# Optimization experiments

Measured on AMD Instinct MI355X. Metric: run time of the kernel, lower is better.

The kernel has to match this reference:

```python
import jax, jax.numpy as jnp
from jax import lax
import numpy as np

N_GROUP = 1024   # number of FPS centroids
N_SAMPLE = 32    # neighbors per ball query
RADIUS = 0.2
BN_EPS = 1e-5    # torch BatchNorm2d default, training-mode batch stats
MLP = [64, 64, 128]
IN_CH = 6        # 3 relative xyz + 3 point features


def setup_inputs() -> dict:
    key = jax.random.key(0)
    ks = jax.random.split(key, 8)
    B, N = 16, 4096
    out = {
        "xyz": jax.random.uniform(ks[0], (B, N, 3), dtype=jnp.float32),
        "point_feature": jax.random.normal(ks[1], (B, N, 3), dtype=jnp.float32),
    }
    last = IN_CH
    for li, oc in enumerate(MLP):
        out[f"w{li}"] = jax.random.normal(ks[2 + li], (oc, last), dtype=jnp.float32) / np.float32(np.sqrt(last))
        out[f"b{li}"] = jnp.zeros((oc,), jnp.float32)
        out[f"g{li}"] = jnp.ones((oc,), jnp.float32)
        out[f"be{li}"] = jnp.zeros((oc,), jnp.float32)
        last = oc
    return out


def _fps(xyz, n_group):
    # Farthest point sampling. xyz: [B, N, 3] -> idx [B, n_group]
    B, N, _ = xyz.shape

    def step(carry, _):
        dist, farthest = carry                      # [B,N], [B]
        centroid = jnp.take_along_axis(xyz, farthest[:, None, None], axis=1)  # [B,1,3]
        d = jnp.sum((xyz - centroid) ** 2, -1)      # [B,N]
        dist = jnp.minimum(dist, d)
        nxt = jnp.argmax(dist, -1).astype(jnp.int32)
        return (dist, nxt), farthest

    init = (jnp.full((B, N), 1e10, xyz.dtype), jnp.zeros((B,), jnp.int32))
    _, idxs = lax.scan(step, init, None, length=n_group)
    return idxs.T                                    # [B, n_group]


def _ball_query(xyz, new_xyz, radius, n_sample):
    # xyz: [B,N,3], new_xyz: [B,S,3] -> idx [B,S,n_sample]
    B, N, _ = xyz.shape
    sqr = jnp.sum((new_xyz[:, :, None, :] - xyz[:, None, :, :]) ** 2, -1)  # [B,S,N]
    idx = jnp.where(sqr > radius * radius, N, jnp.arange(N, dtype=jnp.int32))
    idx = jnp.sort(idx, axis=-1)[:, :, :n_sample]    # closest-index fill like torch impl
    first = idx[:, :, :1]
    return jnp.where(idx == N, first, idx)


def reference(xyz, point_feature, w0, b0, g0, be0, w1, b1, g1, be1, w2, b2, g2, be2):
    B = xyz.shape[0]
    fps_idx = _fps(xyz, N_GROUP)                     # [B,S]
    bi = jnp.arange(B)[:, None]
    new_xyz = xyz[bi, fps_idx]                       # [B,S,3]

    idx = _ball_query(xyz, new_xyz, RADIUS, N_SAMPLE)  # [B,S,K]
    bii = jnp.arange(B)[:, None, None]
    grouped_xyz = xyz[bii, idx] - new_xyz[:, :, None, :]   # [B,S,K,3] centered
    grouped_feat = point_feature[bii, idx]                 # [B,S,K,3]
    x = jnp.concatenate([grouped_xyz, grouped_feat], -1)   # [B,S,K,6]

    # 1x1 Conv2d == per-point linear; BN over all dims but channel (training stats)
    for w, b, g, be in ((w0, b0, g0, be0), (w1, b1, g1, be1), (w2, b2, g2, be2)):
        x = jnp.einsum('bskc,oc->bsko', x, w) + b
        mu = x.mean((0, 1, 2))
        var = x.var((0, 1, 2))
        x = g * (x - mu) * lax.rsqrt(var + BN_EPS) + be
        x = jax.nn.relu(x)

    new_feature = x.max(axis=2)                      # max over n_sample -> [B,S,128]
    return new_xyz, new_feature
```

## Files before the change

kernel.cpp:

```cpp
#include <hip/hip_runtime.h>
#include <hip/hip_bf16.h>

constexpr int BATCH = 16;
constexpr int NPT   = 4096;
constexpr int NGRP  = 1024;
constexpr int NSMP  = 32;
constexpr int NPTS  = BATCH * NGRP * NSMP;
constexpr int PBLK  = 4096;
constexpr int NG    = BATCH * NGRP;

__device__ __forceinline__ float sqd(float dx, float dy, float dz) {
  return __fadd_rn(__fadd_rn(__fmul_rn(dx, dx), __fmul_rn(dy, dy)), __fmul_rn(dz, dz));
}

template <int CTRL, int RM>
__device__ __forceinline__ unsigned long long dpp_lvl(unsigned long long P) {
  const int lo = (int)(unsigned int)P;
  const int hi = (int)(unsigned int)(P >> 32);
  const int tlo = __builtin_amdgcn_update_dpp(lo, lo, CTRL, RM, 0xF, false);
  const int thi = __builtin_amdgcn_update_dpp(hi, hi, CTRL, RM, 0xF, false);
  const unsigned long long T =
      ((unsigned long long)(unsigned int)thi << 32) | (unsigned int)tlo;
  return (T > P) ? T : P;
}

__global__ __launch_bounds__(256) void fps_kernel(const float* __restrict__ xyz,
                                                  float* __restrict__ out) {
  __shared__ float sx[NPT], sy[NPT], sz[NPT];
  __shared__ float cq[NGRP * 3];
  __shared__ unsigned int ex[2][5][4];
  const int b = blockIdx.x;
  const int t = threadIdx.x;
  const float* src = xyz + (size_t)b * NPT * 3;
  for (int i = t; i < NPT; i += 256) {
    sx[i] = src[i * 3 + 0];
    sy[i] = src[i * 3 + 1];
    sz[i] = src[i * 3 + 2];
  }
  __syncthreads();
  float px[16], py[16], pz[16], dist[16];
  #pragma unroll
  for (int j = 0; j < 16; ++j) {
    const int p = j * 256 + t;
    px[j] = sx[p]; py[j] = sy[p]; pz[j] = sz[p];
    dist[j] = 1e10f;
  }
  const int w = t >> 6;
  float cx = sx[0], cy = sy[0], cz = sz[0];
  for (int step = 0; step < NGRP; ++step) {
    if (t == 0) {
      cq[step * 3 + 0] = cx;
      cq[step * 3 + 1] = cy;
      cq[step * 3 + 2] = cz;
    }
    float bestd = -1.0f; int bi = 0x7fffffff;
    #pragma unroll
    for (int j = 0; j < 16; ++j) {
      float d = sqd(px[j] - cx, py[j] - cy, pz[j] - cz);
      d = fminf(dist[j], d);
      dist[j] = d;
      if (d > bestd) { bestd = d; bi = j * 256 + t; }
    }
    const int myidx = bi;
    const unsigned long long myP =
        ((unsigned long long)__float_as_uint(bestd) << 32) |
        (unsigned long long)(unsigned int)~myidx;
    const float mx = sx[myidx], my_ = sy[myidx], mz = sz[myidx];
    unsigned long long P = myP;
    P = dpp_lvl<0xB1, 0xF>(P);
    P = dpp_lvl<0x4E, 0xF>(P);
    P = dpp_lvl<0x141, 0xF>(P);
    P = dpp_lvl<0x140, 0xF>(P);
    P = dpp_lvl<0x142, 0xA>(P);
    P = dpp_lvl<0x143, 0xC>(P);
    const unsigned int flo = (unsigned int)__builtin_amdgcn_readlane((int)(unsigned int)P, 63);
    const unsigned int fhi =
        (unsigned int)__builtin_amdgcn_readlane((int)(unsigned int)(P >> 32), 63);
    const unsigned long long PF = ((unsigned long long)fhi << 32) | flo;
    const int pb = step & 1;
    if (myP == PF) {
      ex[pb][0][w] = fhi;
      ex[pb][1][w] = flo;
      ex[pb][2][w] = __float_as_uint(mx);
      ex[pb][3][w] = __float_as_uint(my_);
      ex[pb][4][w] = __float_as_uint(mz);
    }
    __syncthreads();
    const unsigned int* e = &ex[pb][0][0];
    unsigned long long best = ((unsigned long long)e[0] << 32) | e[4];
    cx = __uint_as_float(e[8]);
    cy = __uint_as_float(e[12]);
    cz = __uint_as_float(e[16]);
    #pragma unroll
    for (int k = 1; k < 4; ++k) {
      const unsigned long long pk_ = ((unsigned long long)e[k] << 32) | e[4 + k];
      if (pk_ > best) {
        best = pk_;
        cx = __uint_as_float(e[8 + k]);
        cy = __uint_as_float(e[12 + k]);
        cz = __uint_as_float(e[16 + k]);
      }
    }
  }
  __syncthreads();
  float* outx = out + (size_t)b * NGRP * 3;
  for (int i = t; i < NGRP * 3; i += 256) outx[i] = cq[i];
}

__global__ __launch_bounds__(256) void ballq_kernel(const float* __restrict__ xyz,
                                                    const float* __restrict__ pf,
                                                    const float* __restrict__ out,
                                                    int* __restrict__ idxg,
                                                    float* __restrict__ part) {
  __shared__ float sx[NPT], sy[NPT], sz[NPT];
  __shared__ int   sel[64 * NSMP];
  __shared__ float cent[64][3];
  const int b = blockIdx.x >> 4;
  const int sub = blockIdx.x & 15;
  const float* src = xyz + (size_t)b * NPT * 3;
  for (int i = threadIdx.x; i < NPT; i += 256) {
    sx[i] = src[i * 3 + 0];
    sy[i] = src[i * 3 + 1];
    sz[i] = src[i * 3 + 2];
  }
  __syncthreads();
  const int lane = threadIdx.x & 63;
  const int w = threadIdx.x >> 6;
  const float R2 = __fmul_rn(0.2f, 0.2f);
  for (int gi = 0; gi < 16; ++gi) {
    const int g = w * 16 + gi;
    const int s = sub * 64 + g;
    const float* c = out + ((size_t)b * NGRP + s) * 3;
    const float nx = c[0], ny = c[1], nz = c[2];
    if (lane == 0) { cent[g][0] = nx; cent[g][1] = ny; cent[g][2] = nz; }
    int* og = idxg + ((size_t)b * NGRP + s) * NSMP;
    int* sg = sel + g * NSMP;
    int cnt = 0, firstP = -1;
    for (int base = 0; base < NPT; base += 64) {
      const int p = base + lane;
      const float dsq = sqd(nx - sx[p], ny - sy[p], nz - sz[p]);
      const bool inr = (dsq <= R2);
      unsigned long long m = __ballot(inr);
      if (firstP < 0 && m) firstP = base + (int)__builtin_ctzll(m);
      const int rank = (int)__popcll(m & ((1ull << lane) - 1ull));
      if (inr) {
        const int pos = cnt + rank;
        if (pos < NSMP) { og[pos] = p; sg[pos] = p; }
      }
      cnt += (int)__popcll(m);
      if (cnt >= NSMP) break;
    }
    if (cnt < NSMP) {
      for (int pos = cnt + lane; pos < NSMP; pos += 64) { og[pos] = firstP; sg[pos] = firstP; }
    }
  }
  __syncthreads();
  float acc[27];
  #pragma unroll
  for (int k = 0; k < 27; ++k) acc[k] = 0.0f;
  const float* pfb = pf + (size_t)b * NPT * 3;
  const int g2 = threadIdx.x >> 2;
  const float c0 = cent[g2][0], c1 = cent[g2][1], c2 = cent[g2][2];
  #pragma unroll
  for (int ii = 0; ii < 8; ++ii) {
    const int si = threadIdx.x * 8 + ii;
    const int i = sel[si];
    float in[6];
    in[0] = sx[i] - c0;
    in[1] = sy[i] - c1;
    in[2] = sz[i] - c2;
    in[3] = pfb[i * 3 + 0];
    in[4] = pfb[i * 3 + 1];
    in[5] = pfb[i * 3 + 2];
    #pragma unroll
    for (int k = 0; k < 6; ++k) acc[k] += in[k];
    int k = 6;
    #pragma unroll
    for (int a = 0; a < 6; ++a)
      #pragma unroll
      for (int bb = a; bb < 6; ++bb) { acc[k] = fmaf(in[a], in[bb], acc[k]); ++k; }
  }
  #pragma unroll
  for (int off = 1; off < 64; off <<= 1) {
    #pragma unroll
    for (int k = 0; k < 27; ++k) acc[k] += __shfl_xor(acc[k], off);
  }
  if (lane == 0) {
    const int slot = blockIdx.x * 4 + w;
    #pragma unroll
    for (int k = 0; k < 27; ++k) part[k * 1024 + slot] = acc[k];
  }
}

__global__ void transpose_w3(const float* __restrict__ w3, float* __restrict__ w3t) {
  const int i = blockIdx.x * 256 + threadIdx.x;
  if (i < 128 * 64) {
    const int o = i >> 6, c = i & 63;
    w3t[c * 128 + o] = w3[i];
  }
}

__device__ __forceinline__ void gather6(const float* __restrict__ xyz, const float* __restrict__ pf,
                                        const float* __restrict__ nxyz, const int* __restrict__ idxg,
                                        int tid, float in[6]) {
  const int g = tid >> 5;
  const int b = g >> 10;
  const int i = idxg[tid];
  const float* P = xyz + ((size_t)b * NPT + i) * 3;
  const float* C = nxyz + (size_t)g * 3;
  in[0] = P[0] - C[0];
  in[1] = P[1] - C[1];
  in[2] = P[2] - C[2];
  const float* F = pf + ((size_t)b * NPT + i) * 3;
  in[3] = F[0]; in[4] = F[1]; in[5] = F[2];
}

__device__ __forceinline__ void layer1h(const float in[6], const float* __restrict__ w1,
                                        const float* __restrict__ b1, const float* __restrict__ ss1,
                                        float h1[64]) {
  #pragma unroll
  for (int o = 0; o < 64; ++o) {
    float a = b1[o];
    #pragma unroll
    for (int cc = 0; cc < 6; ++cc) a = fmaf(in[cc], w1[o * 6 + cc], a);
    h1[o] = fmaxf(0.0f, fmaf(a, ss1[o], ss1[64 + o]));
  }
}

__device__ __forceinline__ void zb_stats64(const float* zb, float* __restrict__ part,
                                           int chbase, int nch, int t, int blk) {
  const int c = t >> 1, h = t & 1;
  const float* row = zb + c * 129 + h * 64;
  float s = 0.0f, q = 0.0f;
  for (int i = 0; i < 64; ++i) {
    const float v = row[i];
    s += v;
    q = fmaf(v, v, q);
  }
  s += __shfl_xor(s, 1);
  q += __shfl_xor(q, 1);
  if (h == 0) {
    part[(size_t)(chbase + c) * PBLK + blk]       = s;
    part[(size_t)(nch + chbase + c) * PBLK + blk] = q;
  }
}

__device__ __forceinline__ void zb_stats_mm(const float* zb, float* __restrict__ part,
                                            float* __restrict__ pmax, float* __restrict__ pmin,
                                            int chbase, int nch, int t, int blk) {
  const int c = t >> 1, h = t & 1;
  const float* row = zb + c * 129 + h * 64;
  float s = 0.0f, q = 0.0f;
  float mx0 = -3.4e38f, mn0 = 3.4e38f, mx1 = -3.4e38f, mn1 = 3.4e38f;
  for (int i = 0; i < 32; ++i) {
    const float v = row[i];
    s += v; q = fmaf(v, v, q);
    mx0 = fmaxf(mx0, v); mn0 = fminf(mn0, v);
  }
  for (int i = 32; i < 64; ++i) {
    const float v = row[i];
    s += v; q = fmaf(v, v, q);
    mx1 = fmaxf(mx1, v); mn1 = fminf(mn1, v);
  }
  s += __shfl_xor(s, 1);
  q += __shfl_xor(q, 1);
  if (h == 0) {
    part[(size_t)(chbase + c) * PBLK + blk]       = s;
    part[(size_t)(nch + chbase + c) * PBLK + blk] = q;
  }
  const size_t g0 = (size_t)blk * 4 + 2 * h;
  pmax[g0 * 128 + chbase + c]       = mx0;
  pmax[(g0 + 1) * 128 + chbase + c] = mx1;
  pmin[g0 * 128 + chbase + c]       = mn0;
  pmin[(g0 + 1) * 128 + chbase + c] = mn1;
}

__global__ __launch_bounds__(256) void momred_kernel(const float* __restrict__ part,
                                                     double* __restrict__ dsum, int n) {
  const int c = blockIdx.x;
  const int t = threadIdx.x;
  double s = 0.0;
  for (int i = t; i < n; i += 256) s += (double)part[c * n + i];
  #pragma unroll
  for (int off = 1; off < 64; off <<= 1) s += __shfl_xor(s, off);
  __shared__ double ls[4];
  const int lane = t & 63, w = t >> 6;
  if (lane == 0) ls[w] = s;
  __syncthreads();
  if (t == 0) dsum[c] = ls[0] + ls[1] + ls[2] + ls[3];
}

__global__ __launch_bounds__(64) void finalize1_kernel(const double* __restrict__ dsum,
                                                       const float* __restrict__ w1,
                                                       const float* __restrict__ b1,
                                                       const float* __restrict__ g,
                                                       const float* __restrict__ be,
                                                       float* __restrict__ ss) {
  __shared__ double sm[27];
  const int t = threadIdx.x;
  if (t < 27) sm[t] = dsum[t];
  __syncthreads();
  const double N = (double)NPTS;
  double wv[6];
  #pragma unroll
  for (int i = 0; i < 6; ++i) wv[i] = (double)w1[t * 6 + i];
  double mean_wx = 0.0;
  #pragma unroll
  for (int i = 0; i < 6; ++i) mean_wx += wv[i] * sm[i];
  mean_wx /= N;
  const double bb = (double)b1[t];
  const double mu = mean_wx + bb;
  double qq = 0.0;
  int k = 6;
  #pragma unroll
  for (int i = 0; i < 6; ++i)
    #pragma unroll
    for (int j = i; j < 6; ++j) {
      qq += (i == j ? 1.0 : 2.0) * wv[i] * wv[j] * (sm[k] / N);
      ++k;
    }
  const double Ez2 = qq + 2.0 * bb * mean_wx + bb * bb;
  const double var = Ez2 - mu * mu;
  const double inv = 1.0 / sqrt(var + 1e-5);
  ss[t]      = (float)((double)g[t] * inv);
  ss[64 + t] = (float)((double)be[t] - (double)g[t] * mu * inv);
}

__global__ __launch_bounds__(256) void reduce_kernel(const float* __restrict__ part, int nblk, int nch,
                                                     const float* __restrict__ g, const float* __restrict__ be,
                                                     float* __restrict__ ss) {
  const int c = blockIdx.x;
  const int t = threadIdx.x;
  double s = 0.0, q = 0.0;
  for (int i = t; i < nblk; i += 256) {
    s += (double)part[(size_t)c * nblk + i];
    q += (double)part[(size_t)(nch + c) * nblk + i];
  }
  #pragma unroll
  for (int off = 1; off < 64; off <<= 1) {
    s += __shfl_xor(s, off);
    q += __shfl_xor(q, off);
  }
  __shared__ double ls[4], lq[4];
  const int lane = t & 63, w = t >> 6;
  if (lane == 0) { ls[w] = s; lq[w] = q; }
  __syncthreads();
  if (t == 0) {
    const double S = ls[0] + ls[1] + ls[2] + ls[3];
    const double Q = lq[0] + lq[1] + lq[2] + lq[3];
    const double n = (double)NPTS;
    const double mu = S / n;
    const double var = Q / n - mu * mu;
    const double inv = 1.0 / sqrt(var + 1e-5);
    ss[c]       = (float)((double)g[c] * inv);
    ss[nch + c] = (float)((double)be[c] - (double)g[c] * mu * inv);
  }
}

__global__ __launch_bounds__(128) void pass2_kernel(const float* __restrict__ xyz, const float* __restrict__ pf,
                                                    const float* __restrict__ nxyz, const int* __restrict__ idxg,
                                                    const float* __restrict__ w1, const float* __restrict__ b1,
                                                    const float* __restrict__ ss1,
                                                    const float* __restrict__ w2, const float* __restrict__ b2,
                                                    float* __restrict__ part,
                                                    __hip_bfloat16* __restrict__ z2c) {
  __shared__ float zb[64 * 129];
  const int t = threadIdx.x;
  const int tid = blockIdx.x * 128 + t;
  float in[6];
  gather6(xyz, pf, nxyz, idxg, tid, in);
  float h1[64];
  layer1h(in, w1, b1, ss1, h1);
  for (int o = 0; o < 64; ++o) {
    float a = b2[o];
    #pragma unroll
    for (int cc = 0; cc < 64; ++cc) a = fmaf(h1[cc], w2[o * 64 + cc], a);
    zb[o * 129 + t] = a;
    if (z2c) z2c[(size_t)o * NPTS + tid] = __float2bfloat16(a);
  }
  __syncthreads();
  zb_stats64(zb, part, 0, 64, t, blockIdx.x);
}

__device__ __forceinline__ void compute_z3(const float* __restrict__ xyz, const float* __restrict__ pf,
                                           const float* __restrict__ nxyz, const int* __restrict__ idxg,
                                           const float* __restrict__ w1, const float* __restrict__ b1,
                                           const float* __restrict__ ss1,
                                           const float* __restrict__ w2, const float* __restrict__ b2,
                                           const float* __restrict__ ss2,
                                           const float* __restrict__ w3t, const float* __restrict__ b3,
                                           const __hip_bfloat16* __restrict__ z2c,
                                           float* shm, int t, int tid, float acc[128]) {
  float* hrow = shm + t * 65;
  if (z2c) {
    #pragma unroll
    for (int o = 0; o < 64; ++o) {
      const float z = __bfloat162float(z2c[(size_t)o * NPTS + tid]);
      hrow[o] = fmaxf(0.0f, fmaf(z, ss2[o], ss2[64 + o]));
    }
  } else {
    float in[6];
    gather6(xyz, pf, nxyz, idxg, tid, in);
    float h1[64];
    layer1h(in, w1, b1, ss1, h1);
    for (int o = 0; o < 64; ++o) {
      float a = b2[o];
      #pragma unroll
      for (int cc = 0; cc < 64; ++cc) a = fmaf(h1[cc], w2[o * 64 + cc], a);
      hrow[o] = fmaxf(0.0f, fmaf(a, ss2[o], ss2[64 + o]));
    }
  }
  #pragma unroll
  for (int o = 0; o < 128; ++o) acc[o] = b3[o];
  for (int cc = 0; cc < 64; ++cc) {
    const float hc = hrow[cc];
    const float* wrow = w3t + cc * 128;
    #pragma unroll
    for (int o = 0; o < 128; ++o) acc[o] = fmaf(hc, wrow[o], acc[o]);
  }
}

__global__ __launch_bounds__(128) void pass3_kernel(const float* __restrict__ xyz, const float* __restrict__ pf,
                                                    const float* __restrict__ nxyz, const int* __restrict__ idxg,
                                                    const float* __restrict__ w1, const float* __restrict__ b1,
                                                    const float* __restrict__ ss1,
                                                    const float* __restrict__ w2, const float* __restrict__ b2,
                                                    const float* __restrict__ ss2,
                                                    const float* __restrict__ w3t, const float* __restrict__ b3,
                                                    const __hip_bfloat16* __restrict__ z2c,
                                                    float* __restrict__ part,
                                                    float* __restrict__ pmax, float* __restrict__ pmin) {
  __shared__ float shm[8320];
  const int t = threadIdx.x;
  const int tid = blockIdx.x * 128 + t;
  float acc[128];
  compute_z3(xyz, pf, nxyz, idxg, w1, b1, ss1, w2, b2, ss2, w3t, b3, z2c, shm, t, tid, acc);
  __syncthreads();
  #pragma unroll
  for (int o = 0; o < 64; ++o) shm[o * 129 + t] = acc[o];
  __syncthreads();
  if (pmax) zb_stats_mm(shm, part, pmax, pmin, 0, 128, t, blockIdx.x);
  else      zb_stats64(shm, part, 0, 128, t, blockIdx.x);
  __syncthreads();
  #pragma unroll
  for (int o = 0; o < 64; ++o) shm[o * 129 + t] = acc[64 + o];
  __syncthreads();
  if (pmax) zb_stats_mm(shm, part, pmax, pmin, 64, 128, t, blockIdx.x);
  else      zb_stats64(shm, part, 64, 128, t, blockIdx.x);
}

__global__ __launch_bounds__(256) void pass4f_kernel(const float* __restrict__ pmax,
                                                     const float* __restrict__ pmin,
                                                     const float* __restrict__ ss3,
                                                     float* __restrict__ outF) {
  const int i = blockIdx.x * 256 + threadIdx.x;
  const int c = i & 127;
  const float a = ss3[c], bb = ss3[128 + c];
  const float z = (a >= 0.0f) ? pmax[i] : pmin[i];
  outF[i] = fmaxf(0.0f, fmaf(z, a, bb));
}

__global__ __launch_bounds__(128) void pass4_kernel(const float* __restrict__ xyz, const float* __restrict__ pf,
                                                    const float* __restrict__ nxyz, const int* __restrict__ idxg,
                                                    const float* __restrict__ w1, const float* __restrict__ b1,
                                                    const float* __restrict__ ss1,
                                                    const float* __restrict__ w2, const float* __restrict__ b2,
                                                    const float* __restrict__ ss2,
                                                    const float* __restrict__ w3t, const float* __restrict__ b3,
                                                    const __hip_bfloat16* __restrict__ z2c,
                                                    const float* __restrict__ ss3,
                                                    float* __restrict__ outF) {
  __shared__ float shm[8320];
  const int t = threadIdx.x;
  const int tid = blockIdx.x * 128 + t;
  float acc[128];
  compute_z3(xyz, pf, nxyz, idxg, w1, b1, ss1, w2, b2, ss2, w3t, b3, z2c, shm, t, tid, acc);
  #pragma unroll
  for (int o = 0; o < 128; ++o)
    acc[o] = fmaxf(0.0f, fmaf(acc[o], ss3[o], ss3[128 + o]));
  __syncthreads();
  const int c4 = t & 63, gp = t >> 6;
  #pragma unroll
  for (int o = 0; o < 64; ++o) shm[o * 129 + t] = acc[o];
  __syncthreads();
  #pragma unroll
  for (int gs = 0; gs < 2; ++gs) {
    const int g = gp * 2 + gs;
    const float* row = shm + c4 * 129 + g * 32;
    float m = row[0];
    for (int i = 1; i < 32; ++i) m = fmaxf(m, row[i]);
    outF[((size_t)blockIdx.x * 4 + g) * 128 + c4] = m;
  }
  __syncthreads();
  #pragma unroll
  for (int o = 0; o < 64; ++o) shm[o * 129 + t] = acc[64 + o];
  __syncthreads();
  #pragma unroll
  for (int gs = 0; gs < 2; ++gs) {
    const int g = gp * 2 + gs;
    const float* row = shm + c4 * 129 + g * 32;
    float m = row[0];
    for (int i = 1; i < 32; ++i) m = fmaxf(m, row[i]);
    outF[((size_t)blockIdx.x * 4 + g) * 128 + 64 + c4] = m;
  }
}

extern "C" void kernel_launch(void* const* d_in, const int* in_sizes, int n_in,
                              void* d_out, int out_size, void* d_ws, size_t ws_size,
                              hipStream_t stream) {
  (void)in_sizes; (void)n_in; (void)out_size;
  const float* xyz = (const float*)d_in[0];
  const float* pf  = (const float*)d_in[1];
  const float* w1  = (const float*)d_in[2];
  const float* b1  = (const float*)d_in[3];
  const float* g1  = (const float*)d_in[4];
  const float* be1 = (const float*)d_in[5];
  const float* w2  = (const float*)d_in[6];
  const float* b2  = (const float*)d_in[7];
  const float* g2  = (const float*)d_in[8];
  const float* be2 = (const float*)d_in[9];
  const float* w3  = (const float*)d_in[10];
  const float* b3  = (const float*)d_in[11];
  const float* g3  = (const float*)d_in[12];
  const float* be3 = (const float*)d_in[13];
  float* out = (float*)d_out;

  int*    idxg = (int*)d_ws;
  float*  p1   = (float*)((char*)d_ws + (size_t)NPTS * 4);
  float*  ss1  = p1 + (size_t)PBLK * 128;
  float*  p2   = ss1 + 128;
  float*  ss2  = p2 + (size_t)PBLK * 128;
  float*  p3   = ss2 + 128;
  float*  ss3  = p3 + (size_t)PBLK * 256;
  float*  w3t  = ss3 + 256;
  double* dsum = (double*)(w3t + 8192);
  float*  pmax = (float*)(dsum + 32);
  float*  pmin = pmax + (size_t)NG * 128;
  __hip_bfloat16* z2c = (__hip_bfloat16*)(pmin + (size_t)NG * 128);
  const size_t needed4 = (size_t)((char*)z2c - (char*)d_ws);
  const size_t needed3 = needed4 + (size_t)NPTS * 64 * sizeof(__hip_bfloat16);
  const bool fast4 = (ws_size >= needed4);
  const bool fast3 = (ws_size >= needed3);
  __hip_bfloat16* z2cp = fast3 ? z2c : nullptr;

  transpose_w3<<<32, 256, 0, stream>>>(w3, w3t);
  fps_kernel<<<BATCH, 256, 0, stream>>>(xyz, out);
  ballq_kernel<<<BATCH * 16, 256, 0, stream>>>(xyz, pf, out, idxg, p1);
  momred_kernel<<<27, 256, 0, stream>>>(p1, dsum, 1024);
  finalize1_kernel<<<1, 64, 0, stream>>>(dsum, w1, b1, g1, be1, ss1);
  pass2_kernel<<<PBLK, 128, 0, stream>>>(xyz, pf, out, idxg, w1, b1, ss1, w2, b2, p2, z2cp);
  reduce_kernel<<<64, 256, 0, stream>>>(p2, PBLK, 64, g2, be2, ss2);
  pass3_kernel<<<PBLK, 128, 0, stream>>>(xyz, pf, out, idxg, w1, b1, ss1, w2, b2, ss2, w3t, b3, z2cp,
                                         p3, fast4 ? pmax : nullptr, fast4 ? pmin : nullptr);
  reduce_kernel<<<128, 256, 0, stream>>>(p3, PBLK, 128, g3, be3, ss3);
  float* outF = out + (size_t)BATCH * NGRP * 3;
  if (fast4) {
    pass4f_kernel<<<(NG * 128) / 256, 256, 0, stream>>>(pmax, pmin, ss3, outF);
  } else {
    pass4_kernel<<<PBLK, 128, 0, stream>>>(xyz, pf, out, idxg, w1, b1, ss1, w2, b2, ss2, w3t, b3,
                                           z2cp, ss3, outF);
  }
}
```

Measured before the change: 1.187 ms.

## Bin FPS points into spatial cells and skip threads whose bounding box cannot improve

The FPS kernel now counting-sorts each batch's points into a 4x4x4 grid so each thread owns 16 spatially contiguous points, tracking their bounding box and original indices. On each step a thread computes a lower bound on its distance to the new centroid and skips the 16-point distance update when that bound cannot lower its current maximum. Ties are broken on original index to preserve argmax semantics. Centroids are written straight to global memory instead of staged through shared memory. This adds setup cost (histogram atomics, scan) and divergence within wavefronts; the skip only saves time if whole wavefronts skip together.

```diff
diff --git a/kernel.cpp b/kernel.cpp
--- a/kernel.cpp
+++ b/kernel.cpp
@@ -27,45 +27,85 @@
 __global__ __launch_bounds__(256) void fps_kernel(const float* __restrict__ xyz,
                                                   float* __restrict__ out) {
   __shared__ float sx[NPT], sy[NPT], sz[NPT];
-  __shared__ float cq[NGRP * 3];
+  __shared__ unsigned short soi[NPT];
+  __shared__ unsigned int hist[64], off[64];
   __shared__ unsigned int ex[2][5][4];
   const int b = blockIdx.x;
   const int t = threadIdx.x;
   const float* src = xyz + (size_t)b * NPT * 3;
-  for (int i = t; i < NPT; i += 256) {
-    sx[i] = src[i * 3 + 0];
-    sy[i] = src[i * 3 + 1];
-    sz[i] = src[i * 3 + 2];
+  if (t < 64) hist[t] = 0;
+  __syncthreads();
+  float mxv[16], myv[16], mzv[16];
+  int myc[16];
+  #pragma unroll
+  for (int j = 0; j < 16; ++j) {
+    const int i = j * 256 + t;
+    const float x = src[i * 3 + 0], y = src[i * 3 + 1], z = src[i * 3 + 2];
+    mxv[j] = x; myv[j] = y; mzv[j] = z;
+    const int cxi = min(3, max(0, (int)(x * 4.0f)));
+    const int cyi = min(3, max(0, (int)(y * 4.0f)));
+    const int czi = min(3, max(0, (int)(z * 4.0f)));
+    myc[j] = cxi * 16 + cyi * 4 + czi;
+    atomicAdd(&hist[myc[j]], 1u);
+  }
+  __syncthreads();
+  if (t == 0) {
+    unsigned int run = 0;
+    for (int c = 0; c < 64; ++c) { off[c] = run; run += hist[c]; }
+  }
+  __syncthreads();
+  #pragma unroll
+  for (int j = 0; j < 16; ++j) {
+    const unsigned int pos = atomicAdd(&off[myc[j]], 1u);
+    sx[pos] = mxv[j]; sy[pos] = myv[j]; sz[pos] = mzv[j];
+    soi[pos] = (unsigned short)(j * 256 + t);
   }
   __syncthreads();
   float px[16], py[16], pz[16], dist[16];
+  int oir[16];
+  float alox = 1e30f, ahix = -1e30f, aloy = 1e30f, ahiy = -1e30f, aloz = 1e30f, ahiz = -1e30f;
   #pragma unroll
   for (int j = 0; j < 16; ++j) {
-    const int p = j * 256 + t;
+    const int p = t * 16 + j;
     px[j] = sx[p]; py[j] = sy[p]; pz[j] = sz[p];
+    oir[j] = (int)soi[p];
     dist[j] = 1e10f;
+    alox = fminf(alox, px[j]); ahix = fmaxf(ahix, px[j]);
+    aloy = fminf(aloy, py[j]); ahiy = fmaxf(ahiy, py[j]);
+    aloz = fminf(aloz, pz[j]); ahiz = fmaxf(ahiz, pz[j]);
   }
   const int w = t >> 6;
-  float cx = sx[0], cy = sy[0], cz = sz[0];
+  float cx = src[0], cy = src[1], cz = src[2];
+  float myMax = 1e10f;
+  float bestd = -1.0f; int bpos = 0; int bestO = 0x7fffffff;
+  float* outx = out + (size_t)b * NGRP * 3;
   for (int step = 0; step < NGRP; ++step) {
     if (t == 0) {
-      cq[step * 3 + 0] = cx;
-      cq[step * 3 + 1] = cy;
-      cq[step * 3 + 2] = cz;
-    }
-    float bestd = -1.0f; int bi = 0x7fffffff;
-    #pragma unroll
-    for (int j = 0; j < 16; ++j) {
-      float d = sqd(px[j] - cx, py[j] - cy, pz[j] - cz);
-      d = fminf(dist[j], d);
-      dist[j] = d;
-      if (d > bestd) { bestd = d; bi = j * 256 + t; }
-    }
-    const int myidx = bi;
+      outx[step * 3 + 0] = cx;
+      outx[step * 3 + 1] = cy;
+      outx[step * 3 + 2] = cz;
+    }
+    const float ddx = fmaxf(0.0f, fmaxf(alox - cx, cx - ahix));
+    const float ddy = fmaxf(0.0f, fmaxf(aloy - cy, cy - ahiy));
+    const float ddz = fmaxf(0.0f, fmaxf(aloz - cz, cz - ahiz));
+    const float lb = sqd(ddx, ddy, ddz);
+    if (0.999f * lb < myMax) {
+      bestd = -1.0f; bestO = 0x7fffffff; bpos = 0;
+      #pragma unroll
+      for (int j = 0; j < 16; ++j) {
+        float d = sqd(px[j] - cx, py[j] - cy, pz[j] - cz);
+        d = fminf(dist[j], d);
+        dist[j] = d;
+        if (d > bestd || (d == bestd && oir[j] < bestO)) {
+          bestd = d; bestO = oir[j]; bpos = t * 16 + j;
+        }
+      }
+      myMax = bestd;
+    }
     const unsigned long long myP =
         ((unsigned long long)__float_as_uint(bestd) << 32) |
-        (unsigned long long)(unsigned int)~myidx;
-    const float mx = sx[myidx], my_ = sy[myidx], mz = sz[myidx];
+        (unsigned long long)(unsigned int)~bestO;
+    const float mx = sx[bpos], my_ = sy[bpos], mz = sz[bpos];
     unsigned long long P = myP;
     P = dpp_lvl<0xB1, 0xF>(P);
     P = dpp_lvl<0x4E, 0xF>(P);
@@ -102,9 +142,6 @@
       }
     }
   }
-  __syncthreads();
-  float* outx = out + (size_t)b * NGRP * 3;
-  for (int i = t; i < NGRP * 3; i += 256) outx[i] = cq[i];
 }
 
 __global__ __launch_bounds__(256) void ballq_kernel(const float* __restrict__ xyz,
```

After: 2.081 ms. +75.3%, slower.
